# Performance work log

Measured on AMD Instinct MI355X. Metric: run time of the kernel, lower is better.

Reference implementation:

```python
import jax, jax.numpy as jnp
import numpy as np

EPS = 1e-6
K_HOPS = 2  # SGConv K


def setup_inputs() -> dict:
    key = jax.random.key(0)
    k1, k2, k3, k4 = jax.random.split(key, 4)
    B, Kk, C, T = 32, 8, 64, 250
    E, H = 4096, 128
    x = jax.random.normal(k1, (B, Kk, C, T), dtype=jnp.float32)
    edge_index = jax.random.randint(k2, (2, E), 0, C, dtype=jnp.int64)
    edge_weights = jax.random.uniform(k3, (E,), dtype=jnp.float32)
    W = jax.random.normal(k4, (H, Kk * T), dtype=jnp.float32) * 0.02
    b = jnp.zeros((H,), dtype=jnp.float32)
    return {"x": x, "edge_index": edge_index, "edge_weights": edge_weights, "W": W, "b": b}


def reference(x, edge_index, edge_weights, W, b):
    B, Kk, C, T = x.shape
    N = C  # nodes
    x = x.reshape(B, N, Kk * T)  # (B, N, F)

    # clamp non-positive edge weights to epsilon (mirrors in-place .data clamp)
    w = jnp.where(edge_weights <= 0, EPS, edge_weights)

    # gcn_norm with self loops (fill value 1.0)
    src, dst = edge_index[0], edge_index[1]
    loop = jnp.arange(N, dtype=edge_index.dtype)
    src = jnp.concatenate([src, loop])
    dst = jnp.concatenate([dst, loop])
    w = jnp.concatenate([w, jnp.ones((N,), w.dtype)])
    deg = jnp.zeros((N,), w.dtype).at[dst].add(w)
    dinv = jnp.where(deg > 0, deg ** -0.5, jnp.zeros_like(deg))
    norm = dinv[src] * w * dinv[dst]  # (E+N,)

    # K hops of gather -> weight -> scatter-add aggregation
    for _ in range(K_HOPS):
        msg = x[:, src, :] * norm[None, :, None]        # (B, E+N, F)
        x = jnp.zeros_like(x).at[:, dst, :].add(msg)    # (B, N, F)

    # final linear: y = x @ W^T + b
    return jnp.einsum('bnf,hf->bnh', x, W) + b
```

## Files before the change

### kernel.cpp

```cpp
#include <hip/hip_runtime.h>
#include <hip/hip_bf16.h>

#define EPSW 1e-6f

typedef __attribute__((ext_vector_type(4))) float floatx4;
typedef __attribute__((ext_vector_type(4))) unsigned int uintx4;
typedef __attribute__((ext_vector_type(8))) short shortx8;

__device__ __forceinline__ unsigned short f2bf(float f) {
    unsigned int u = __float_as_uint(f);
    u = (u + 0x7fffu + ((u >> 16) & 1u)) >> 16;
    return (unsigned short)u;
}

__device__ __forceinline__ unsigned int pk2(float lo, float hi) {
    return (unsigned int)f2bf(lo) | ((unsigned int)f2bf(hi) << 16);
}

__device__ __forceinline__ shortx8 pk8s(floatx4 a, floatx4 b) {
    union { uintx4 u; shortx8 s; } r;
    r.u.x = pk2(a.x, a.y); r.u.y = pk2(a.z, a.w);
    r.u.z = pk2(b.x, b.y); r.u.w = pk2(b.z, b.w);
    return r.s;
}

__global__ __launch_bounds__(256) void mbuild(const int* __restrict__ ei,
                                              const float* __restrict__ ew,
                                              float* __restrict__ Mt) {
    __shared__ float sA[4224];
    const int bm = blockIdx.x;
    const int t  = threadIdx.x;
    float* A    = sA;
    float* deg  = A + 4096;
    float* dinv = deg + 64;
    if (t < 64) deg[t] = 1.0f;
    for (int i = t; i < 4096; i += 256) A[i] = 0.0f;
    __syncthreads();
    const int* srcp = ei;
    const int* dstp = ei + 4096;
#pragma unroll
    for (int i = 0; i < 16; ++i) {
        const int e = i * 256 + t;
        float w = ew[e];
        w = (w <= 0.0f) ? EPSW : w;
        atomicAdd(&deg[dstp[e]], w);
    }
    __syncthreads();
    if (t < 64) dinv[t] = 1.0f / sqrtf(deg[t]);
    __syncthreads();
#pragma unroll
    for (int i = 0; i < 16; ++i) {
        const int e = i * 256 + t;
        float w = ew[e];
        w = (w <= 0.0f) ? EPSW : w;
        const int s = srcp[e], d = dstp[e];
        atomicAdd(&A[d * 64 + s], dinv[s] * w * dinv[d]);
    }
    if (t < 64) atomicAdd(&A[t * 64 + t], dinv[t] * dinv[t]);
    __syncthreads();
    const int c  = t & 63;
    const int rr = t >> 6;
    float s0 = 0.f, s1 = 0.f, s2 = 0.f, s3 = 0.f;
#pragma unroll 8
    for (int k = 0; k < 64; ++k) {
        const float akc = A[k * 64 + c];
        const float* an = A + (bm * 16 + rr * 4) * 64 + k;
        s0 += an[0]   * akc;
        s1 += an[64]  * akc;
        s2 += an[128] * akc;
        s3 += an[192] * akc;
    }
    float* mo = Mt + c * 64 + bm * 16 + rr * 4;
    mo[0] = s0; mo[1] = s1; mo[2] = s2; mo[3] = s3;
}

__global__ __launch_bounds__(512) void gcn_fused(
        const float* __restrict__ x,
        const float* __restrict__ W,
        const float* __restrict__ Mtg,
        const float* __restrict__ bias,
        float* __restrict__ y) {
    __shared__ __align__(16) float lds[8 * 1088 + 1088 + 4096];
    float* zpart = lds;
    float* zs    = lds + 8 * 1088;
    float* Ms    = zs + 1088;

    const int t     = threadIdx.x;
    const int bid   = blockIdx.x;
    const int hs    = bid >> 5;
    const int batch = bid & 31;
    const int rbase = batch * 64;
    const int hbase = hs * 16;

    const int wave = t >> 6, lane = t & 63;
    const int m = lane & 15, q = lane >> 4;

    const float* xr0 = x + (size_t)(rbase + m) * 2000;
    const float* wr  = W + (size_t)(hbase + m) * 2000;

    floatx4 acc[4];
#pragma unroll
    for (int rt = 0; rt < 4; ++rt) acc[rt] = (floatx4){0.f, 0.f, 0.f, 0.f};

    floatx4 fA[3][4][2];
    floatx4 fB[3][2];

#define LOADK(i_)                                                             \
    {                                                                         \
        const int s_ = (i_) % 3;                                              \
        const int c_ = wave + (i_) * 8;                      \
        const int k_ = c_ * 32 + q * 8;                                       \
        if (k_ < 2000) {                                                      \
            _Pragma("unroll")                                                 \
            for (int rt_ = 0; rt_ < 4; ++rt_) {                               \
                const float* p_ = xr0 + rt_ * 32000 + k_;                     \
                fA[s_][rt_][0] = *(const floatx4*)p_;                         \
                fA[s_][rt_][1] = *(const floatx4*)(p_ + 4);                   \
            }                                                                 \
            fB[s_][0] = *(const floatx4*)(wr + k_);                           \
            fB[s_][1] = *(const floatx4*)(wr + k_ + 4);                       \
        } else {                                                              \
            _Pragma("unroll")                                                 \
            for (int rt_ = 0; rt_ < 4; ++rt_)                                 \
                fA[s_][rt_][0] = fA[s_][rt_][1] =                             \
                    (floatx4){0.f, 0.f, 0.f, 0.f};                            \
            fB[s_][0] = fB[s_][1] = (floatx4){0.f, 0.f, 0.f, 0.f};            \
        }                                                                     \
    }

    LOADK(0);
    LOADK(1);
#pragma unroll
    for (int i = 0; i < 8; ++i) {
        const int s = i % 3;
        shortx8 af[4];
#pragma unroll
        for (int rt = 0; rt < 4; ++rt)
            af[rt] = pk8s(fA[s][rt][0], fA[s][rt][1]);
        const shortx8 bf = pk8s(fB[s][0], fB[s][1]);
        if (i < 6) LOADK(i + 2);
#pragma unroll
        for (int rt = 0; rt < 4; ++rt)
            acc[rt] = __builtin_amdgcn_mfma_f32_16x16x32_bf16(
                af[rt], bf, acc[rt], 0, 0, 0);
    }
#undef LOADK

    const floatx4 msr0 = *(const floatx4*)(Mtg + t * 8);
    const floatx4 msr1 = *(const floatx4*)(Mtg + t * 8 + 4);

    float* zw = zpart + wave * 1088;
#pragma unroll
    for (int rt = 0; rt < 4; ++rt)
#pragma unroll
        for (int v = 0; v < 4; ++v)
            zw[(rt * 16 + q * 4 + v) * 17 + m] = acc[rt][v];
    __syncthreads();

#pragma unroll
    for (int i = 0; i < 2; ++i) {
        const int idx = i * 512 + t;
        const int row = idx >> 4, hh = idx & 15;
        float s = 0.0f;
#pragma unroll
        for (int w = 0; w < 8; ++w) s += zpart[w * 1088 + row * 17 + hh];
        zs[row * 17 + hh] = s;
    }
    *(floatx4*)(Ms + t * 8)     = msr0;
    *(floatx4*)(Ms + t * 8 + 4) = msr1;
    __syncthreads();

    const int h  = t & 15;
    const int n0 = (t >> 4) * 2;
    float s0 = 0.0f, s1 = 0.0f;
#pragma unroll 8
    for (int mm = 0; mm < 64; ++mm) {
        const float zv = zs[mm * 17 + h];
        s0 += Ms[mm * 64 + n0]     * zv;
        s1 += Ms[mm * 64 + n0 + 1] * zv;
    }
    const float bv = bias[hbase + h];
    float* yp = y + (size_t)batch * 8192 + (size_t)n0 * 128 + hbase + h;
    yp[0]   = bv + s0;
    yp[128] = bv + s1;
}

extern "C" void kernel_launch(void* const* d_in, const int* in_sizes, int n_in,
                              void* d_out, int out_size, void* d_ws, size_t ws_size,
                              hipStream_t stream) {
    const float* x    = (const float*)d_in[0];
    const int*   ei   = (const int*)d_in[1];
    const float* ew   = (const float*)d_in[2];
    const float* W    = (const float*)d_in[3];
    const float* bias = (const float*)d_in[4];
    float* y = (float*)d_out;

    float* Mt = (float*)d_ws;

    mbuild<<<4, 256, 0, stream>>>(ei, ew, Mt);
    gcn_fused<<<256, 512, 0, stream>>>(x, W, Mt, bias, y);
}
```

Baseline: 98.52 us.

## Fuse propagation-matrix build into main kernel and stage GEMM operands via LDS

Removes the separate mbuild launch. Each of the 256 blocks now redundantly builds the normalized adjacency and its square (M = A^2) in shared memory, overlapping that work with the first global prefetches of x and W. The GEMM main loop is restructured so threads load coalesced rows, pack them to bf16 and write them into double-buffered LDS staging, and MFMA operands are then read back from LDS. This saves a kernel launch and the global round trip for M, at the cost of repeated per-block atomics and matrix-square work, extra barriers, and much larger LDS use (~136 KB), which limits occupancy to one block per CU.

```diff
diff --git a/kernel.cpp b/kernel.cpp
--- a/kernel.cpp
+++ b/kernel.cpp
@@ -17,73 +17,23 @@
     return (unsigned int)f2bf(lo) | ((unsigned int)f2bf(hi) << 16);
 }
 
-__device__ __forceinline__ shortx8 pk8s(floatx4 a, floatx4 b) {
-    union { uintx4 u; shortx8 s; } r;
-    r.u.x = pk2(a.x, a.y); r.u.y = pk2(a.z, a.w);
-    r.u.z = pk2(b.x, b.y); r.u.w = pk2(b.z, b.w);
-    return r.s;
-}
-
-__global__ __launch_bounds__(256) void mbuild(const int* __restrict__ ei,
-                                              const float* __restrict__ ew,
-                                              float* __restrict__ Mt) {
-    __shared__ float sA[4224];
-    const int bm = blockIdx.x;
-    const int t  = threadIdx.x;
-    float* A    = sA;
-    float* deg  = A + 4096;
-    float* dinv = deg + 64;
-    if (t < 64) deg[t] = 1.0f;
-    for (int i = t; i < 4096; i += 256) A[i] = 0.0f;
-    __syncthreads();
-    const int* srcp = ei;
-    const int* dstp = ei + 4096;
-#pragma unroll
-    for (int i = 0; i < 16; ++i) {
-        const int e = i * 256 + t;
-        float w = ew[e];
-        w = (w <= 0.0f) ? EPSW : w;
-        atomicAdd(&deg[dstp[e]], w);
-    }
-    __syncthreads();
-    if (t < 64) dinv[t] = 1.0f / sqrtf(deg[t]);
-    __syncthreads();
-#pragma unroll
-    for (int i = 0; i < 16; ++i) {
-        const int e = i * 256 + t;
-        float w = ew[e];
-        w = (w <= 0.0f) ? EPSW : w;
-        const int s = srcp[e], d = dstp[e];
-        atomicAdd(&A[d * 64 + s], dinv[s] * w * dinv[d]);
-    }
-    if (t < 64) atomicAdd(&A[t * 64 + t], dinv[t] * dinv[t]);
-    __syncthreads();
-    const int c  = t & 63;
-    const int rr = t >> 6;
-    float s0 = 0.f, s1 = 0.f, s2 = 0.f, s3 = 0.f;
-#pragma unroll 8
-    for (int k = 0; k < 64; ++k) {
-        const float akc = A[k * 64 + c];
-        const float* an = A + (bm * 16 + rr * 4) * 64 + k;
-        s0 += an[0]   * akc;
-        s1 += an[64]  * akc;
-        s2 += an[128] * akc;
-        s3 += an[192] * akc;
-    }
-    float* mo = Mt + c * 64 + bm * 16 + rr * 4;
-    mo[0] = s0; mo[1] = s1; mo[2] = s2; mo[3] = s3;
-}
-
-__global__ __launch_bounds__(512) void gcn_fused(
+__device__ __forceinline__ uintx4 pk8(floatx4 a, floatx4 b) {
+    uintx4 r;
+    r.x = pk2(a.x, a.y); r.y = pk2(a.z, a.w);
+    r.z = pk2(b.x, b.y); r.w = pk2(b.z, b.w);
+    return r;
+}
+
+__global__ __launch_bounds__(512) void gcn_all(
         const float* __restrict__ x,
         const float* __restrict__ W,
-        const float* __restrict__ Mtg,
+        const int* __restrict__ ei,
+        const float* __restrict__ ew,
         const float* __restrict__ bias,
         float* __restrict__ y) {
-    __shared__ __align__(16) float lds[8 * 1088 + 1088 + 4096];
-    float* zpart = lds;
-    float* zs    = lds + 8 * 1088;
-    float* Ms    = zs + 1088;
+    __shared__ float Ms[4096];
+    __shared__ __align__(16) unsigned char stg[2][40960];
+    __shared__ float red[9792];
 
     const int t     = threadIdx.x;
     const int bid   = blockIdx.x;
@@ -95,61 +45,121 @@
     const int wave = t >> 6, lane = t & 63;
     const int m = lane & 15, q = lane >> 4;
 
-    const float* xr0 = x + (size_t)(rbase + m) * 2000;
-    const float* wr  = W + (size_t)(hbase + m) * 2000;
-
     floatx4 acc[4];
 #pragma unroll
     for (int rt = 0; rt < 4; ++rt) acc[rt] = (floatx4){0.f, 0.f, 0.f, 0.f};
 
-    floatx4 fA[3][4][2];
-    floatx4 fB[3][2];
-
-#define LOADK(i_)                                                             \
+    floatx4 fx[2][4][2];
+    floatx4 fw[2][2];
+
+#define LOADS(s_)                                                             \
     {                                                                         \
-        const int s_ = (i_) % 3;                                              \
-        const int c_ = wave + (i_) * 8;                      \
-        const int k_ = c_ * 32 + q * 8;                                       \
-        if (k_ < 2000) {                                                      \
-            _Pragma("unroll")                                                 \
-            for (int rt_ = 0; rt_ < 4; ++rt_) {                               \
-                const float* p_ = xr0 + rt_ * 32000 + k_;                     \
-                fA[s_][rt_][0] = *(const floatx4*)p_;                         \
-                fA[s_][rt_][1] = *(const floatx4*)(p_ + 4);                   \
+        const int p_ = (s_) & 1;                                              \
+        _Pragma("unroll")                                                     \
+        for (int j_ = 0; j_ < 4; ++j_) {                                      \
+            const int k_ = (s_) * 256 + (j_ * 8 + (t & 7)) * 8;               \
+            if (k_ < 2000) {                                                  \
+                const float* px_ =                                            \
+                    x + (size_t)(rbase + (t >> 3)) * 2000 + k_;               \
+                fx[p_][j_][0] = *(const floatx4*)px_;                         \
+                fx[p_][j_][1] = *(const floatx4*)(px_ + 4);                   \
+            } else {                                                          \
+                fx[p_][j_][0] = fx[p_][j_][1] =                               \
+                    (floatx4){0.f, 0.f, 0.f, 0.f};                            \
             }                                                                 \
-            fB[s_][0] = *(const floatx4*)(wr + k_);                           \
-            fB[s_][1] = *(const floatx4*)(wr + k_ + 4);                       \
+        }                                                                     \
+        const int kw_ = (s_) * 256 + (t & 31) * 8;                            \
+        if (kw_ < 2000) {                                                     \
+            const float* pw_ =                                                \
+                W + (size_t)(hbase + (t >> 5)) * 2000 + kw_;                  \
+            fw[p_][0] = *(const floatx4*)pw_;                                 \
+            fw[p_][1] = *(const floatx4*)(pw_ + 4);                           \
         } else {                                                              \
-            _Pragma("unroll")                                                 \
-            for (int rt_ = 0; rt_ < 4; ++rt_)                                 \
-                fA[s_][rt_][0] = fA[s_][rt_][1] =                             \
-                    (floatx4){0.f, 0.f, 0.f, 0.f};                            \
-            fB[s_][0] = fB[s_][1] = (floatx4){0.f, 0.f, 0.f, 0.f};            \
+            fw[p_][0] = fw[p_][1] = (floatx4){0.f, 0.f, 0.f, 0.f};            \
         }                                                                     \
     }
 
-    LOADK(0);
-    LOADK(1);
-#pragma unroll
-    for (int i = 0; i < 8; ++i) {
-        const int s = i % 3;
+#define WRITES(s_)                                                            \
+    {                                                                         \
+        const int p_ = (s_) & 1;                                              \
+        unsigned char* sb_ = stg[p_];                                         \
+        _Pragma("unroll")                                                     \
+        for (int j_ = 0; j_ < 4; ++j_)                                        \
+            *(uintx4*)(sb_ + ((j_ * 8 + (t & 7)) * 64 + (t >> 3)) * 16) =     \
+                pk8(fx[p_][j_][0], fx[p_][j_][1]);                            \
+        *(uintx4*)(sb_ + 32768 + ((t & 31) * 16 + (t >> 5)) * 16) =           \
+            pk8(fw[p_][0], fw[p_][1]);                                        \
+    }
+
+    LOADS(0);
+    LOADS(1);
+
+    {
+        float* A    = red;
+        float* deg  = red + 4096;
+        float* dinv = deg + 64;
+        if (t < 64) deg[t] = 1.0f;
+        for (int i = t; i < 4096; i += 512) A[i] = 0.0f;
+        __syncthreads();
+        const int* srcp = ei;
+        const int* dstp = ei + 4096;
+#pragma unroll
+        for (int i = 0; i < 8; ++i) {
+            const int e = i * 512 + t;
+            float w = ew[e];
+            w = (w <= 0.0f) ? EPSW : w;
+            atomicAdd(&deg[dstp[e]], w);
+        }
+        __syncthreads();
+        if (t < 64) dinv[t] = 1.0f / sqrtf(deg[t]);
+        __syncthreads();
+#pragma unroll
+        for (int i = 0; i < 8; ++i) {
+            const int e = i * 512 + t;
+            float w = ew[e];
+            w = (w <= 0.0f) ? EPSW : w;
+            const int s = srcp[e], d = dstp[e];
+            atomicAdd(&A[d * 64 + s], dinv[s] * w * dinv[d]);
+        }
+        if (t < 64) atomicAdd(&A[t * 64 + t], dinv[t] * dinv[t]);
+        __syncthreads();
+        const int c   = t & 63;
+        const int n0m = (t >> 6) * 8;
+        float s[8];
+#pragma unroll
+        for (int j = 0; j < 8; ++j) s[j] = 0.0f;
+#pragma unroll 8
+        for (int k = 0; k < 64; ++k) {
+            const float akc = A[k * 64 + c];
+#pragma unroll
+            for (int j = 0; j < 8; ++j) s[j] += A[(n0m + j) * 64 + k] * akc;
+        }
+#pragma unroll
+        for (int j = 0; j < 8; ++j) Ms[c * 64 + n0m + j] = s[j];
+        __syncthreads();
+    }
+
+#pragma unroll
+    for (int s = 0; s < 8; ++s) {
+        WRITES(s);
+        if (s < 6) LOADS(s + 2);
+        __syncthreads();
+        const unsigned char* sb = stg[s & 1];
+        const int kg = wave * 4 + q;
         shortx8 af[4];
 #pragma unroll
         for (int rt = 0; rt < 4; ++rt)
-            af[rt] = pk8s(fA[s][rt][0], fA[s][rt][1]);
-        const shortx8 bf = pk8s(fB[s][0], fB[s][1]);
-        if (i < 6) LOADK(i + 2);
+            af[rt] = *(const shortx8*)(sb + (kg * 64 + rt * 16 + m) * 16);
+        const shortx8 bf = *(const shortx8*)(sb + 32768 + (kg * 16 + m) * 16);
 #pragma unroll
         for (int rt = 0; rt < 4; ++rt)
             acc[rt] = __builtin_amdgcn_mfma_f32_16x16x32_bf16(
                 af[rt], bf, acc[rt], 0, 0, 0);
     }
-#undef LOADK
-
-    const floatx4 msr0 = *(const floatx4*)(Mtg + t * 8);
-    const floatx4 msr1 = *(const floatx4*)(Mtg + t * 8 + 4);
-
-    float* zw = zpart + wave * 1088;
+#undef LOADS
+#undef WRITES
+
+    float* zw = red + wave * 1088;
 #pragma unroll
     for (int rt = 0; rt < 4; ++rt)
 #pragma unroll
@@ -157,17 +167,16 @@
             zw[(rt * 16 + q * 4 + v) * 17 + m] = acc[rt][v];
     __syncthreads();
 
+    float* zs = red + 8704;
 #pragma unroll
     for (int i = 0; i < 2; ++i) {
         const int idx = i * 512 + t;
         const int row = idx >> 4, hh = idx & 15;
-        float s = 0.0f;
-#pragma unroll
-        for (int w = 0; w < 8; ++w) s += zpart[w * 1088 + row * 17 + hh];
-        zs[row * 17 + hh] = s;
-    }
-    *(floatx4*)(Ms + t * 8)     = msr0;
-    *(floatx4*)(Ms + t * 8 + 4) = msr1;
+        float ssum = 0.0f;
+#pragma unroll
+        for (int w = 0; w < 8; ++w) ssum += red[w * 1088 + row * 17 + hh];
+        zs[row * 17 + hh] = ssum;
+    }
     __syncthreads();
 
     const int h  = t & 15;
@@ -195,8 +204,5 @@
     const float* bias = (const float*)d_in[4];
     float* y = (float*)d_out;
 
-    float* Mt = (float*)d_ws;
-
-    mbuild<<<4, 256, 0, stream>>>(ei, ew, Mt);
-    gcn_fused<<<256, 512, 0, stream>>>(x, W, Mt, bias, y);
-}
+    gcn_all<<<256, 512, 0, stream>>>(x, W, ei, ew, bias, y);
+}
```

Result: no change. 97.83 us (-0.7%).
